# Kernel optimization log

Hardware: AMD Instinct MI355X
Metric: run time of the kernel (lower is better)

## Reference

```python
import jax, jax.numpy as jnp
import numpy as np

VDE, VEN = 30000, 30000
D, H, M = 620, 1000, 1000
B, S, T = 32, 20, 20  # T = decoder steps = y.shape[1]-1


def _lstm(xe, Wih, Whh, b):
    """Single-layer LSTM, batch_first. xe: [B,L,D] -> [B,L,H]. PyTorch gate order i,f,g,o.
    (b = b_ih + b_hh; mathematically identical to PyTorch's two biases.)"""
    Bn = xe.shape[0]
    Hn = Whh.shape[1]
    xp = jnp.einsum('bld,gd->blg', xe, Wih) + b  # [B,L,4H]

    def step(carry, xt):
        h, c = carry
        gates = xt + h @ Whh.T
        i, f, g, o = jnp.split(gates, 4, axis=-1)
        c = jax.nn.sigmoid(f) * c + jax.nn.sigmoid(i) * jnp.tanh(g)
        h = jax.nn.sigmoid(o) * jnp.tanh(c)
        return (h, c), h

    init = (jnp.zeros((Bn, Hn), xe.dtype), jnp.zeros((Bn, Hn), xe.dtype))
    _, hs = jax.lax.scan(step, init, jnp.swapaxes(xp, 0, 1))
    return jnp.swapaxes(hs, 0, 1)


def setup_inputs() -> dict:
    key = jax.random.key(0)
    ks = jax.random.split(key, 24)

    def w(k, shape, s=0.05):
        return jax.random.normal(k, shape, jnp.float32) * s

    return {
        'x': jax.random.randint(ks[0], (B, S), 0, VDE),
        'y': jax.random.randint(ks[1], (B, T + 1), 0, VEN),
        'emb_de': w(ks[2], (VDE, D)),
        'emb_en': w(ks[3], (VEN, D)),
        'enc_Wih': w(ks[4], (4 * H, D)), 'enc_Whh': w(ks[5], (4 * H, H)), 'enc_b': jnp.zeros((4 * H,), jnp.float32),
        'dec_Wih': w(ks[6], (4 * H, D)), 'dec_Whh': w(ks[7], (4 * H, H)), 'dec_b': jnp.zeros((4 * H,), jnp.float32),
        'Wa_w': w(ks[8], (H, H)), 'Wa_b': jnp.zeros((H,), jnp.float32),
        'Ua_w': w(ks[9], (H, H)), 'Ua_b': jnp.zeros((H,), jnp.float32),
        'Va_w': w(ks[10], (H,)), 'Va_b': jnp.zeros((), jnp.float32),
        'U_w': w(ks[11], (2 * M, H)), 'U_b': jnp.zeros((2 * M,), jnp.float32),
        'V_w': w(ks[12], (2 * M, D)), 'V_b': jnp.zeros((2 * M,), jnp.float32),
        'C_w': w(ks[13], (2 * M, H)), 'C_b': jnp.zeros((2 * M,), jnp.float32),
        'W_w': w(ks[14], (VEN, M)), 'W_b': jnp.zeros((VEN,), jnp.float32),
    }


def reference(x, y, emb_de, emb_en, enc_Wih, enc_Whh, enc_b,
              dec_Wih, dec_Whh, dec_b, Wa_w, Wa_b, Ua_w, Ua_b, Va_w, Va_b,
              U_w, U_b, V_w, V_b, C_w, C_b, W_w, W_b):
    e_de = emb_de[x]                 # [B,S,D]
    e_en = emb_en[y]                 # [B,T+1,D]
    enc_h = _lstm(e_de, enc_Wih, enc_Whh, enc_b)          # [B,S,H]
    dec_h = _lstm(e_en[:, :-1], dec_Wih, dec_Whh, dec_b)  # [B,T,H]

    # Bahdanau additive attention (fused broadcast-add + tanh + Va)
    Wa = jnp.einsum('bth,gh->btg', dec_h, Wa_w) + Wa_b    # [B,T,H]
    Ua = jnp.einsum('bsh,gh->bsg', enc_h, Ua_w) + Ua_b    # [B,S,H]
    scores = jnp.einsum('bsth,h->bst', jnp.tanh(Ua[:, :, None, :] + Wa[:, None, :, :]), Va_w) + Va_b  # [B,S,T]

    attn = jax.nn.softmax(scores, axis=1)                 # softmax over source positions
    context = jnp.einsum('bst,bsh->bth', attn, enc_h)     # [B,T,H]

    # deep-output maxout layer, batched over all t
    u = (jnp.einsum('bth,gh->btg', dec_h, U_w) + U_b
         + jnp.einsum('btd,gd->btg', e_en[:, :-1], V_w) + V_b
         + jnp.einsum('bth,gh->btg', context, C_w) + C_b)  # [B,T,2M]
    t_max = jnp.max(u.reshape(B, T, M, 2), axis=-1)        # [B,T,M]

    logits = jnp.einsum('btm,vm->btv', t_max, W_w) + W_b   # [B,T,Ven]
    logp = jax.nn.log_softmax(logits, axis=-1)
    labels = y[:, 1:]                                      # [B,T]
    nll = -jnp.take_along_axis(logp, labels[:, :, None], axis=-1)[..., 0]  # [B,T]
    # original: sum over t of NLLLoss(mean over batch)
    loss = jnp.sum(jnp.mean(nll, axis=0))
    return loss
```

## Files before the change

### kernel.cpp

```cpp
#include <hip/hip_runtime.h>
#include <math.h>

#define VEN_  30000
#define Dd    620
#define Hh    1000
#define Gg    4000
#define Mm    1000
#define Bb    32
#define Ss    20
#define Tt    20
#define NST   470

typedef __attribute__((ext_vector_type(8))) short short8b;
typedef __attribute__((ext_vector_type(4))) float f32x4;

typedef __attribute__((address_space(1))) void GASV;
typedef __attribute__((address_space(3))) void LASV;
#define GLOAD_LDS16(g, l) \
    __builtin_amdgcn_global_load_lds((GASV*)(const void*)(g), (LASV*)(void*)(l), 16, 0, 0)

__device__ __forceinline__ float sigf(float x) { return 1.0f / (1.0f + __expf(-x)); }
__device__ __forceinline__ ushort f2bf(float f) {
    unsigned u = __float_as_uint(f);
    u = (u + 0x7fffu + ((u >> 16) & 1u)) >> 16;
    return (ushort)u;
}
__device__ __forceinline__ float bf2f(ushort u) { return __uint_as_float(((unsigned)u) << 16); }
__device__ __forceinline__ short8b cvt8(float4 a, float4 b) {
    ushort v[8];
    v[0] = f2bf(a.x); v[1] = f2bf(a.y); v[2] = f2bf(a.z); v[3] = f2bf(a.w);
    v[4] = f2bf(b.x); v[5] = f2bf(b.y); v[6] = f2bf(b.z); v[7] = f2bf(b.w);
    return *(short8b*)v;
}

__global__ void conv_bf16(const float* __restrict__ in, int K,
                          ushort* __restrict__ out, int ostride, int kp8, int total) {
    int idx = blockIdx.x * 256 + threadIdx.x;
    if (idx >= total) return;
    int rr = idx / kp8, c8 = (idx % kp8) * 8;
    const float* src = in + (size_t)rr * K + c8;
    short8b o;
    if (c8 + 7 < K) {
        o = cvt8(*(const float4*)src, *(const float4*)(src + 4));
    } else {
        ushort v[8];
        #pragma unroll
        for (int j = 0; j < 8; ++j) v[j] = (c8 + j < K) ? f2bf(src[j]) : (ushort)0;
        o = *(short8b*)v;
    }
    *(short8b*)&out[(size_t)rr * ostride + c8] = o;
}

struct ConvJob { const float* src; ushort* dst; int K; int ostride; int kp8; unsigned end; };
struct ConvJobs { ConvJob j[9]; };

__global__ void conv_multi(ConvJobs jobs, unsigned total) {
    unsigned v = blockIdx.x * 256 + threadIdx.x;
    if (v >= total) return;
    int ji = 0;
    while (v >= jobs.j[ji].end) ++ji;
    unsigned base = ji ? jobs.j[ji - 1].end : 0;
    unsigned local = v - base;
    const ConvJob J = jobs.j[ji];
    int rr = local / J.kp8, c8 = (local % J.kp8) * 8;
    const float* src = J.src + (size_t)rr * J.K + c8;
    short8b o;
    if (c8 + 7 < J.K) {
        o = cvt8(*(const float4*)src, *(const float4*)(src + 4));
    } else {
        ushort w[8];
        #pragma unroll
        for (int j = 0; j < 8; ++j) w[j] = (c8 + j < J.K) ? f2bf(src[j]) : (ushort)0;
        o = *(short8b*)w;
    }
    *(short8b*)&J.dst[(size_t)rr * J.ostride + c8] = o;
}

__global__ void gather2(const float* __restrict__ embA, const int* __restrict__ tokA,
                        int strA, ushort* __restrict__ outA, int osA,
                        const float* __restrict__ embB, const int* __restrict__ tokB,
                        int strB, ushort* __restrict__ outB, int osB) {
    int idx = blockIdx.x * 256 + threadIdx.x;
    if (idx >= Bb * Tt * 80) return;
    const float* emb; const int* toks; int tstride; ushort* out; int ostride;
    if (blockIdx.y == 0) { emb = embA; toks = tokA; tstride = strA; out = outA; ostride = osA; }
    else                 { emb = embB; toks = tokB; tstride = strB; out = outB; ostride = osB; }
    int row = idx / 80, c8 = (idx % 80) * 8;
    int b = row / Tt, t = row % Tt;
    int tok = toks[b * tstride + t];
    const float* src = emb + (size_t)tok * Dd + c8;
    short8b o;
    if (c8 + 7 < Dd) {
        o = cvt8(*(const float4*)src, *(const float4*)(src + 4));
    } else {
        ushort v[8];
        #pragma unroll
        for (int j = 0; j < 8; ++j) v[j] = (c8 + j < Dd) ? f2bf(src[j]) : (ushort)0;
        o = *(short8b*)v;
    }
    *(short8b*)&out[(size_t)row * ostride + c8] = o;
}

struct GemmArgs {
    const ushort* A; int lda;
    const ushort* B; int ldb;
    const float* bias; const float* bias2; const float* bias3;
    float* C; int ldc;
    float* pm; float* ps; ushort* Cb;
    int M, N, Kp, MT;
};

template <int MODE>
__device__ __forceinline__ void gemm_body(ushort* As, ushort* Bs, const GemmArgs g) {
    const int tid = threadIdx.x;
    const int w = tid >> 6, lane = tid & 63;
    const int wm = w >> 1, wn = w & 1;
    const int lhi = lane >> 4, llo = lane & 15;

    int nblk = gridDim.x;
    int q = nblk >> 3, r = nblk & 7;
    int xcd = blockIdx.x & 7, lo = blockIdx.x >> 3;
    int wg = ((xcd < r) ? xcd * (q + 1) : r * (q + 1) + (xcd - r) * q) + lo;
    int mt = wg % g.MT, nt = wg / g.MT;
    const int row0 = mt * 128, col0 = nt * 128;

    const int lr8 = lane >> 3;
    const int cs = (lane & 7) ^ lr8;
    const ushort* pA[4];
    const ushort* pB[4];
    #pragma unroll
    for (int qq = 0; qq < 4; ++qq) {
        int seg = w + qq * 4;
        int ra = row0 + seg * 8 + lr8; if (ra > g.M - 1) ra = g.M - 1;
        int rb = col0 + seg * 8 + lr8; if (rb > g.N - 1) rb = g.N - 1;
        pA[qq] = g.A + (size_t)ra * g.lda + cs * 8;
        pB[qq] = g.B + (size_t)rb * g.ldb + cs * 8;
    }

    f32x4 acc[4][4] = {};

    #pragma unroll
    for (int qq = 0; qq < 4; ++qq) {
        int seg = w + qq * 4;
        GLOAD_LDS16(pA[qq], (char*)As + (seg << 10));
        GLOAD_LDS16(pB[qq], (char*)Bs + (seg << 10));
    }
    __syncthreads();

    int cur = 0;
    for (int kk = 0; kk < g.Kp; kk += 64) {
        if (kk + 64 < g.Kp) {
            int nb = (cur ^ 1) << 14;
            #pragma unroll
            for (int qq = 0; qq < 4; ++qq) {
                int seg = w + qq * 4;
                GLOAD_LDS16(pA[qq] + kk + 64, (char*)As + nb + (seg << 10));
                GLOAD_LDS16(pB[qq] + kk + 64, (char*)Bs + nb + (seg << 10));
            }
        }
        const char* curA = (const char*)As + (cur << 14);
        const char* curB = (const char*)Bs + (cur << 14);
        #pragma unroll
        for (int ks = 0; ks < 2; ++ks) {
            short8b af[4], bg[4];
            #pragma unroll
            for (int i = 0; i < 4; ++i) {
                int Ra = wm * 64 + i * 16 + llo;
                int ca = (ks * 4 + lhi) ^ (Ra & 7);
                af[i] = *(const short8b*)(curA + Ra * 128 + (ca << 4));
                int Rb = wn * 64 + i * 16 + llo;
                int cbs = (ks * 4 + lhi) ^ (Rb & 7);
                bg[i] = *(const short8b*)(curB + Rb * 128 + (cbs << 4));
            }
            #pragma unroll
            for (int i = 0; i < 4; ++i)
                #pragma unroll
                for (int j = 0; j < 4; ++j)
                    acc[i][j] = __builtin_amdgcn_mfma_f32_16x16x32_bf16(af[i], bg[j], acc[i][j], 0, 0, 0);
        }
        __syncthreads();
        cur ^= 1;
    }

    if (MODE == 0) {
        #pragma unroll
        for (int i = 0; i < 4; ++i) {
            #pragma unroll
            for (int reg = 0; reg < 4; ++reg) {
                int row = row0 + wm * 64 + i * 16 + lhi * 4 + reg;
                if (row >= g.M) continue;
                #pragma unroll
                for (int j = 0; j < 4; ++j) {
                    int col = col0 + wn * 64 + j * 16 + llo;
                    if (col < g.N)
                        g.C[(size_t)row * g.ldc + col] = acc[i][j][reg] + (g.bias ? g.bias[col] : 0.f);
                }
            }
        }
    } else if (MODE == 1) {
        #pragma unroll
        for (int i = 0; i < 4; ++i) {
            #pragma unroll
            for (int reg = 0; reg < 4; ++reg) {
                int row = row0 + wm * 64 + i * 16 + lhi * 4 + reg;
                float vals[4], vmax = -1e30f;
                #pragma unroll
                for (int j = 0; j < 4; ++j) {
                    int col = col0 + wn * 64 + j * 16 + llo;
                    vals[j] = (col < g.N) ? (acc[i][j][reg] + g.bias[col]) : -1e30f;
                    vmax = fmaxf(vmax, vals[j]);
                }
                #pragma unroll
                for (int off = 8; off; off >>= 1) vmax = fmaxf(vmax, __shfl_xor(vmax, off, 16));
                float se = 0.f;
                #pragma unroll
                for (int j = 0; j < 4; ++j) {
                    int col = col0 + wn * 64 + j * 16 + llo;
                    if (col < g.N) se += __expf(vals[j] - vmax);
                }
                #pragma unroll
                for (int off = 8; off; off >>= 1) se += __shfl_xor(se, off, 16);
                if (llo == 0 && row < g.M) {
                    g.pm[(size_t)row * NST + nt * 2 + wn] = vmax;
                    g.ps[(size_t)row * NST + nt * 2 + wn] = se;
                }
            }
        }
    } else {
        #pragma unroll
        for (int i = 0; i < 4; ++i) {
            #pragma unroll
            for (int reg = 0; reg < 4; ++reg) {
                int row = row0 + wm * 64 + i * 16 + lhi * 4 + reg;
                #pragma unroll
                for (int j = 0; j < 4; ++j) {
                    int col = col0 + wn * 64 + j * 16 + llo;
                    int cc = col < g.N ? col : 0;
                    float bv = g.bias[cc] + (g.bias2 ? g.bias2[cc] : 0.f) + (g.bias3 ? g.bias3[cc] : 0.f);
                    float v = acc[i][j][reg] + bv;
                    float o = fmaxf(v, __shfl_xor(v, 1));
                    if (((llo & 1) == 0) && row < g.M && col + 1 < g.N) {
                        int m = col >> 1;
                        g.C[(size_t)row * g.ldc + m] = o;
                        g.Cb[(size_t)row * 1024 + m] = f2bf(o);
                    }
                }
            }
        }
    }
}

template <int MODE>
__global__ __launch_bounds__(256) void gemm_one(GemmArgs g) {
    __shared__ __align__(16) ushort As[2 * 128 * 64];
    __shared__ __align__(16) ushort Bs[2 * 128 * 64];
    gemm_body<MODE>(As, Bs, g);
}

__global__ __launch_bounds__(256) void gemm_pair(GemmArgs g0, GemmArgs g1) {
    __shared__ __align__(16) ushort As[2 * 128 * 64];
    __shared__ __align__(16) ushort Bs[2 * 128 * 64];
    if (blockIdx.y == 0) gemm_body<0>(As, Bs, g0);
    else                 gemm_body<0>(As, Bs, g1);
}

__global__ __launch_bounds__(512) void lstm_all(
    const float* __restrict__ xpE, const float* __restrict__ xpD,
    const ushort* __restrict__ WE, const ushort* __restrict__ WD,
    ushort* __restrict__ hE, ushort* __restrict__ hD,
    int strideE, int strideD, unsigned* __restrict__ flags)
{
    __shared__ float gsm[8][32][16];
    const int which = blockIdx.y;
    const float* xp = which ? xpD : xpE;
    const ushort* Whh = which ? WD : WE;
    ushort* hs = which ? hD : hE;
    const int hstride = which ? strideD : strideE;
    unsigned* fl = flags + which * 64;

    const int tid = threadIdx.x;
    const int wave = tid >> 6, l = tid & 63;
    const int g = wave & 3, half = wave >> 2;
    const int lhi = l >> 4, llo = l & 15;
    const int j0 = blockIdx.x * 16;
    const int jc = (j0 + llo < Hh) ? (j0 + llo) : (Hh - 1);
    const int kbase = half * 512;
    const ushort* wp = Whh + (size_t)(g * Hh + jc) * 1024 + kbase + lhi * 8;

    short8b wreg[16];
    #pragma unroll
    for (int kk = 0; kk < 16; ++kk) wreg[kk] = *(const short8b*)(wp + kk * 32);

    const int ub = tid >> 4, ujj = tid & 15;
    const int ujw = j0 + ujj;
    const float* xpr = xp + (size_t)ub * Tt * Gg;
    float creg = 0.f;

    for (int t = 0; t < Tt; ++t) {
        f32x4 acc0 = {0.f, 0.f, 0.f, 0.f};
        f32x4 acc1 = {0.f, 0.f, 0.f, 0.f};
        if (t > 0) {
            const ushort* h0p = hs + ((size_t)llo * Tt + (t - 1)) * hstride + kbase + lhi * 8;
            const ushort* h1p = hs + ((size_t)(llo + 16) * Tt + (t - 1)) * hstride + kbase + lhi * 8;
            short8b a0r[4], a1r[4];
            #pragma unroll
            for (int pp = 0; pp < 4; ++pp) {
                a0r[pp] = *(const short8b*)(h0p + pp * 32);
                a1r[pp] = *(const short8b*)(h1p + pp * 32);
            }
            #pragma unroll
            for (int kk = 0; kk < 16; ++kk) {
                short8b a0 = a0r[kk & 3], a1 = a1r[kk & 3];
                if (kk + 4 < 16) {
                    a0r[kk & 3] = *(const short8b*)(h0p + (kk + 4) * 32);
                    a1r[kk & 3] = *(const short8b*)(h1p + (kk + 4) * 32);
                }
                acc0 = __builtin_amdgcn_mfma_f32_16x16x32_bf16(a0, wreg[kk], acc0, 0, 0, 0);
                acc1 = __builtin_amdgcn_mfma_f32_16x16x32_bf16(a1, wreg[kk], acc1, 0, 0, 0);
            }
        }
        #pragma unroll
        for (int reg = 0; reg < 4; ++reg) {
            gsm[wave][lhi * 4 + reg][llo]      = acc0[reg];
            gsm[wave][16 + lhi * 4 + reg][llo] = acc1[reg];
        }
        __syncthreads();
        {
            const float* xq = xpr + (size_t)t * Gg;
            float hn = 0.f;
            if (ujw < Hh) {
                float vi = gsm[0][ub][ujj] + gsm[4][ub][ujj] + xq[ujw];
                float vf = gsm[1][ub][ujj] + gsm[5][ub][ujj] + xq[Hh + ujw];
                float vg = gsm[2][ub][ujj] + gsm[6][ub][ujj] + xq[2 * Hh + ujw];
                float vo = gsm[3][ub][ujj] + gsm[7][ub][ujj] + xq[3 * Hh + ujw];
                creg = sigf(vf) * creg + sigf(vi) * tanhf(vg);
                hn = sigf(vo) * tanhf(creg);
            }
            unsigned mine = f2bf(hn);
            unsigned other = (unsigned)__shfl_xor((int)mine, 1);
            if (((ujj & 1) == 0) && ujw + 1 < Hh + 1 && ujw < Hh) {
                unsigned pk = (other << 16) | (mine & 0xFFFFu);
                unsigned* dst = (unsigned*)&hs[((size_t)ub * Tt + t) * hstride + ujw];
                __hip_atomic_store(dst, pk, __ATOMIC_RELAXED, __HIP_MEMORY_SCOPE_SYSTEM);
            }
        }
        if (t + 1 < Tt) {
            __syncthreads();
            if (tid == 0)
                __hip_atomic_store(&fl[blockIdx.x], (unsigned)(t + 1),
                                   __ATOMIC_RELAXED, __HIP_MEMORY_SCOPE_SYSTEM);
            if (tid < 64) {
                unsigned tgt = (unsigned)(t + 1);
                while (true) {
                    unsigned v = (tid < 63)
                        ? __hip_atomic_load(&fl[tid], __ATOMIC_RELAXED, __HIP_MEMORY_SCOPE_SYSTEM)
                        : tgt;
                    if (__all(v >= tgt)) break;
                    __builtin_amdgcn_s_sleep(1);
                }
            }
            __syncthreads();
        }
    }
}

__global__ __launch_bounds__(256) void attn_scores(
    const float* __restrict__ Ua, const float* __restrict__ Wa,
    const float* __restrict__ Va_w, const float* __restrict__ Va_b,
    float* __restrict__ scores)
{
    int wave = (blockIdx.x * 256 + threadIdx.x) >> 6;
    int lane = threadIdx.x & 63;
    if (wave >= Bb * Ss * Tt) return;
    int b = wave / (Ss * Tt);
    int rem = wave % (Ss * Tt);
    int s = rem / Tt, t = rem % Tt;
    const float* ua = Ua + (size_t)(b * Ss + s) * Hh;
    const float* wa = Wa + (size_t)(b * Tt + t) * Hh;
    float acc = 0.f;
    for (int h = lane; h < Hh; h += 64)
        acc += tanhf(ua[h] + wa[h]) * Va_w[h];
    #pragma unroll
    for (int off = 32; off; off >>= 1) acc += __shfl_xor(acc, off, 64);
    if (lane == 0) scores[(size_t)(b * Ss + s) * Tt + t] = acc + Va_b[0];
}

__global__ __launch_bounds__(256) void softmax_context(
    const float* __restrict__ scores, const ushort* __restrict__ enc_hb,
    ushort* __restrict__ ctx_out, int ostride)
{
    __shared__ float w[Ss];
    int b = blockIdx.x / Tt, t = blockIdx.x % Tt;
    if (threadIdx.x == 0) {
        float sc[Ss];
        float mx = -1e30f;
        for (int s = 0; s < Ss; ++s) {
            sc[s] = scores[(size_t)(b * Ss + s) * Tt + t];
            mx = fmaxf(mx, sc[s]);
        }
        float sum = 0.f;
        for (int s = 0; s < Ss; ++s) { float e = __expf(sc[s] - mx); w[s] = e; sum += e; }
        float inv = 1.f / sum;
        for (int s = 0; s < Ss; ++s) w[s] *= inv;
    }
    __syncthreads();
    for (int h = threadIdx.x; h < Hh; h += 256) {
        float acc = 0.f;
        #pragma unroll
        for (int s = 0; s < Ss; ++s)
            acc += w[s] * bf2f(enc_hb[((size_t)b * Ss + s) * 1024 + h]);
        ctx_out[(size_t)(b * Tt + t) * ostride + h] = f2bf(acc);
    }
}

__global__ __launch_bounds__(256) void nll_kernel(
    const float* __restrict__ pm, const float* __restrict__ ps,
    const float* __restrict__ tmax, const float* __restrict__ Ww,
    const float* __restrict__ Wb, const int* __restrict__ y,
    float* __restrict__ nll)
{
    __shared__ float sm[4];
    int row = blockIdx.x;
    int tid = threadIdx.x;
    float mx = -1e30f;
    for (int i = tid; i < NST; i += 256) mx = fmaxf(mx, pm[(size_t)row * NST + i]);
    #pragma unroll
    for (int off = 32; off; off >>= 1) mx = fmaxf(mx, __shfl_xor(mx, off, 64));
    if ((tid & 63) == 0) sm[tid >> 6] = mx;
    __syncthreads();
    mx = fmaxf(fmaxf(sm[0], sm[1]), fmaxf(sm[2], sm[3]));
    __syncthreads();
    float s = 0.f;
    for (int i = tid; i < NST; i += 256)
        s += ps[(size_t)row * NST + i] * __expf(pm[(size_t)row * NST + i] - mx);
    #pragma unroll
    for (int off = 32; off; off >>= 1) s += __shfl_xor(s, off, 64);
    if ((tid & 63) == 0) sm[tid >> 6] = s;
    __syncthreads();
    s = sm[0] + sm[1] + sm[2] + sm[3];
    __syncthreads();
    int b = row / Tt, t = row % Tt;
    int lab = y[b * (Tt + 1) + t + 1];
    float d = 0.f;
    for (int m = tid; m < Mm; m += 256)
        d += tmax[(size_t)row * Mm + m] * Ww[(size_t)lab * Mm + m];
    #pragma unroll
    for (int off = 32; off; off >>= 1) d += __shfl_xor(d, off, 64);
    if ((tid & 63) == 0) sm[tid >> 6] = d;
    __syncthreads();
    d = sm[0] + sm[1] + sm[2] + sm[3] + Wb[lab];
    if (tid == 0) nll[row] = (mx + logf(s)) - d;
}

__global__ void loss_kernel(const float* __restrict__ nll, float* __restrict__ out) {
    __shared__ float sm[4];
    float s = 0.f;
    for (int i = threadIdx.x; i < Bb * Tt; i += 256) s += nll[i];
    #pragma unroll
    for (int off = 32; off; off >>= 1) s += __shfl_xor(s, off, 64);
    if ((threadIdx.x & 63) == 0) sm[threadIdx.x >> 6] = s;
    __syncthreads();
    if (threadIdx.x == 0) out[0] = (sm[0] + sm[1] + sm[2] + sm[3]) / (float)Bb;
}

extern "C" void kernel_launch(void* const* d_in, const int* in_sizes, int n_in,
                              void* d_out, int out_size, void* d_ws, size_t ws_size,
                              hipStream_t stream)
{
    const int* x = (const int*)d_in[0];
    const int* y = (const int*)d_in[1];
    const float* emb_de  = (const float*)d_in[2];
    const float* emb_en  = (const float*)d_in[3];
    const float* enc_Wih = (const float*)d_in[4];
    const float* enc_Whh = (const float*)d_in[5];
    const float* enc_b   = (const float*)d_in[6];
    const float* dec_Wih = (const float*)d_in[7];
    const float* dec_Whh = (const float*)d_in[8];
    const float* dec_b   = (const float*)d_in[9];
    const float* Wa_w = (const float*)d_in[10];
    const float* Wa_b = (const float*)d_in[11];
    const float* Ua_w = (const float*)d_in[12];
    const float* Ua_b = (const float*)d_in[13];
    const float* Va_w = (const float*)d_in[14];
    const float* Va_b = (const float*)d_in[15];
    const float* U_w  = (const float*)d_in[16];
    const float* U_b  = (const float*)d_in[17];
    const float* V_w  = (const float*)d_in[18];
    const float* V_b  = (const float*)d_in[19];
    const float* C_w  = (const float*)d_in[20];
    const float* C_b  = (const float*)d_in[21];
    const float* W_w  = (const float*)d_in[22];
    const float* W_b  = (const float*)d_in[23];

    char* base = (char*)d_ws;
    size_t off = 0;
    auto alloc = [&](size_t bytes) { char* p = base + off; off += (bytes + 255) & ~(size_t)255; return p; };

    float*  xp_enc   = (float*)alloc(640ull * 4000 * 4);
    float*  xp_dec   = (float*)alloc(640ull * 4000 * 4);
    float*  Wa       = (float*)alloc(640ull * 1000 * 4);
    float*  Ua       = (float*)alloc(640ull * 1000 * 4);
    float*  scores   = (float*)alloc((size_t)Bb * Ss * Tt * 4);
    float*  pm       = (float*)alloc(640ull * NST * 4);
    float*  ps       = (float*)alloc(640ull * NST * 4);
    float*  nll      = (float*)alloc(640ull * 4);
    ushort* e_de_b   = (ushort*)alloc(640ull * 640 * 2);
    ushort* A_cat    = (ushort*)alloc(640ull * 2688 * 2);
    ushort* hs_enc_b = (ushort*)alloc(640ull * 1024 * 2);
    unsigned* flags  = (unsigned*)alloc(512);
    ushort* whh_enc_b= (ushort*)alloc(4000ull * 1024 * 2);
    ushort* whh_dec_b= (ushort*)alloc(4000ull * 1024 * 2);
    ushort* wbig     = (ushort*)alloc(30000ull * 1024 * 2);
    ushort* Wcat_b   = (ushort*)alloc(2000ull * 2688 * 2);
    ushort* Wa_w_b   = (ushort*)alloc(1000ull * 1024 * 2);
    ushort* Ua_w_b   = (ushort*)alloc(1000ull * 1024 * 2);

    ushort* wih_enc_b = wbig;
    ushort* wih_dec_b = wbig + 4000ull * 640;
    ushort* W_w_b     = wbig;

    float*  tmax   = xp_enc + 640ull * 2000;
    ushort* tmax_b = (ushort*)xp_dec;

    dim3 blk(256);

    hipMemsetAsync(A_cat, 0, 640ull * 2688 * 2 + 640ull * 1024 * 2 + 512, stream);

    ConvJobs jobs;
    unsigned acc = 0;
    auto J = [&](int i, const float* s, ushort* d, int K, int ostr, int kp8, int R) {
        acc += (unsigned)R * kp8;
        jobs.j[i] = ConvJob{s, d, K, ostr, kp8, acc};
    };
    J(0, enc_Whh, whh_enc_b, 1000, 1024, 128, 4000);
    J(1, dec_Whh, whh_dec_b, 1000, 1024, 128, 4000);
    J(2, enc_Wih, wih_enc_b,  620,  640,  80, 4000);
    J(3, dec_Wih, wih_dec_b,  620,  640,  80, 4000);
    J(4, Wa_w,    Wa_w_b,    1000, 1024, 128, 1000);
    J(5, Ua_w,    Ua_w_b,    1000, 1024, 128, 1000);
    J(6, U_w,     Wcat_b,          1000, 2688, 128, 2000);
    J(7, V_w,     Wcat_b + 1024,    620, 2688,  80, 2000);
    J(8, C_w,     Wcat_b + 1664,   1000, 2688, 128, 2000);
    conv_multi<<<dim3((acc + 255) / 256), blk, 0, stream>>>(jobs, acc);

    gather2<<<dim3(200, 2), blk, 0, stream>>>(emb_de, x, Ss, e_de_b, 640,
                                              emb_en, y, Tt + 1, A_cat + 1024, 2688);

    GemmArgs ge = {e_de_b, 640, wih_enc_b, 640, enc_b, nullptr, nullptr,
                   xp_enc, 4000, nullptr, nullptr, nullptr, 640, 4000, 640, 5};
    GemmArgs gd = {A_cat + 1024, 2688, wih_dec_b, 640, dec_b, nullptr, nullptr,
                   xp_dec, 4000, nullptr, nullptr, nullptr, 640, 4000, 640, 5};
    gemm_pair<<<dim3(160, 2), blk, 0, stream>>>(ge, gd);

    conv_bf16<<<dim3(15000), blk, 0, stream>>>(W_w, 1000, W_w_b, 1024, 128, 30000 * 128);

    lstm_all<<<dim3(63, 2), dim3(512), 0, stream>>>(
        xp_enc, xp_dec, whh_enc_b, whh_dec_b, hs_enc_b, A_cat, 1024, 2688, flags);

    GemmArgs gw = {A_cat, 2688, Wa_w_b, 1024, Wa_b, nullptr, nullptr,
                   Wa, 1000, nullptr, nullptr, nullptr, 640, 1000, 1024, 5};
    GemmArgs gu = {hs_enc_b, 1024, Ua_w_b, 1024, Ua_b, nullptr, nullptr,
                   Ua, 1000, nullptr, nullptr, nullptr, 640, 1000, 1024, 5};
    gemm_pair<<<dim3(40, 2), blk, 0, stream>>>(gw, gu);

    attn_scores<<<dim3(3200), blk, 0, stream>>>(Ua, Wa, Va_w, Va_b, scores);
    softmax_context<<<dim3(640), blk, 0, stream>>>(scores, hs_enc_b, A_cat + 1664, 2688);

    hipMemsetAsync(tmax_b, 0, 640ull * 1024 * 2, stream);

    GemmArgs gm = {A_cat, 2688, Wcat_b, 2688, U_b, V_b, C_b,
                   tmax, 1000, nullptr, nullptr, tmax_b, 640, 2000, 2688, 5};
    gemm_one<2><<<dim3(80), blk, 0, stream>>>(gm);

    GemmArgs gl = {tmax_b, 1024, W_w_b, 1024, W_b, nullptr, nullptr,
                   nullptr, 0, pm, ps, nullptr, 640, VEN_, 1024, 5};
    gemm_one<1><<<dim3(1175), blk, 0, stream>>>(gl);

    nll_kernel<<<dim3(640), blk, 0, stream>>>(pm, ps, tmax, W_w, W_b, y, nll);
    loss_kernel<<<dim3(1), blk, 0, stream>>>(nll, (float*)d_out);
}
```

Measured before the change: 514.3 us.

## Overlap W_w bf16 conversion with LSTM recurrence inside one launch

Removes the standalone conv_bf16 launch. The fp32-to-bf16 conversion of the large output projection W_w is folded into lstm_all as extra worker blocks (6 of every 8 blocks), so it runs alongside the latency-bound recurrent blocks instead of before them. It also prefetches the xp gate inputs before the MFMA work, reads h through agent-scope relaxed atomic loads, and narrows the store and flag atomics from system to agent scope to make cross-block syncs cheaper. The risk is that the conversion blocks compete with the spin-waiting recurrence blocks for bandwidth and CU slots, and residency of all recurrence blocks now depends on the 504-block grid scheduling.

```diff
diff --git a/kernel.cpp b/kernel.cpp
--- a/kernel.cpp
+++ b/kernel.cpp
@@ -31,24 +31,6 @@
     v[0] = f2bf(a.x); v[1] = f2bf(a.y); v[2] = f2bf(a.z); v[3] = f2bf(a.w);
     v[4] = f2bf(b.x); v[5] = f2bf(b.y); v[6] = f2bf(b.z); v[7] = f2bf(b.w);
     return *(short8b*)v;
-}
-
-__global__ void conv_bf16(const float* __restrict__ in, int K,
-                          ushort* __restrict__ out, int ostride, int kp8, int total) {
-    int idx = blockIdx.x * 256 + threadIdx.x;
-    if (idx >= total) return;
-    int rr = idx / kp8, c8 = (idx % kp8) * 8;
-    const float* src = in + (size_t)rr * K + c8;
-    short8b o;
-    if (c8 + 7 < K) {
-        o = cvt8(*(const float4*)src, *(const float4*)(src + 4));
-    } else {
-        ushort v[8];
-        #pragma unroll
-        for (int j = 0; j < 8; ++j) v[j] = (c8 + j < K) ? f2bf(src[j]) : (ushort)0;
-        o = *(short8b*)v;
-    }
-    *(short8b*)&out[(size_t)rr * ostride + c8] = o;
 }
 
 struct ConvJob { const float* src; ushort* dst; int K; int ostride; int kp8; unsigned end; };
@@ -264,14 +246,39 @@
     else                 gemm_body<0>(As, Bs, g1);
 }
 
+union HQ { unsigned long long q[2]; short8b v; };
+
 __global__ __launch_bounds__(512) void lstm_all(
     const float* __restrict__ xpE, const float* __restrict__ xpD,
     const ushort* __restrict__ WE, const ushort* __restrict__ WD,
     ushort* __restrict__ hE, ushort* __restrict__ hD,
-    int strideE, int strideD, unsigned* __restrict__ flags)
+    int strideE, int strideD, unsigned* __restrict__ flags,
+    const float* __restrict__ Ww, ushort* __restrict__ Wwb)
 {
+    const int role = blockIdx.x & 7;
+    const int chunk = blockIdx.x >> 3;
+    if (role != 0 && role != 4) {
+        int wid = chunk * 6 + (role < 4 ? role - 1 : role - 2);
+        const int total = 30000 * 128;
+        for (int idx = wid * 512 + (int)threadIdx.x; idx < total; idx += 378 * 512) {
+            int rr = idx >> 7, c8 = (idx & 127) * 8;
+            const float* src = Ww + (size_t)rr * 1000 + c8;
+            short8b o;
+            if (c8 + 7 < 1000) {
+                o = cvt8(*(const float4*)src, *(const float4*)(src + 4));
+            } else {
+                ushort v[8];
+                #pragma unroll
+                for (int j = 0; j < 8; ++j) v[j] = (c8 + j < 1000) ? f2bf(src[j]) : (ushort)0;
+                o = *(short8b*)v;
+            }
+            *(short8b*)&Wwb[(size_t)rr * 1024 + c8] = o;
+        }
+        return;
+    }
+
     __shared__ float gsm[8][32][16];
-    const int which = blockIdx.y;
+    const int which = role >> 2;
     const float* xp = which ? xpD : xpE;
     const ushort* Whh = which ? WD : WE;
     ushort* hs = which ? hD : hE;
@@ -282,7 +289,7 @@
     const int wave = tid >> 6, l = tid & 63;
     const int g = wave & 3, half = wave >> 2;
     const int lhi = l >> 4, llo = l & 15;
-    const int j0 = blockIdx.x * 16;
+    const int j0 = chunk * 16;
     const int jc = (j0 + llo < Hh) ? (j0 + llo) : (Hh - 1);
     const int kbase = half * 512;
     const ushort* wp = Whh + (size_t)(g * Hh + jc) * 1024 + kbase + lhi * 8;
@@ -297,23 +304,35 @@
     float creg = 0.f;
 
     for (int t = 0; t < Tt; ++t) {
+        float xq0 = 0.f, xq1 = 0.f, xq2 = 0.f, xq3 = 0.f;
+        if (ujw < Hh) {
+            const float* xq = xpr + (size_t)t * Gg;
+            xq0 = xq[ujw]; xq1 = xq[Hh + ujw]; xq2 = xq[2 * Hh + ujw]; xq3 = xq[3 * Hh + ujw];
+        }
+
         f32x4 acc0 = {0.f, 0.f, 0.f, 0.f};
         f32x4 acc1 = {0.f, 0.f, 0.f, 0.f};
         if (t > 0) {
-            const ushort* h0p = hs + ((size_t)llo * Tt + (t - 1)) * hstride + kbase + lhi * 8;
-            const ushort* h1p = hs + ((size_t)(llo + 16) * Tt + (t - 1)) * hstride + kbase + lhi * 8;
-            short8b a0r[4], a1r[4];
+            const unsigned long long* h0q = (const unsigned long long*)
+                (hs + ((size_t)llo * Tt + (t - 1)) * hstride + kbase + lhi * 8);
+            const unsigned long long* h1q = (const unsigned long long*)
+                (hs + ((size_t)(llo + 16) * Tt + (t - 1)) * hstride + kbase + lhi * 8);
+            HQ a0r[4], a1r[4];
             #pragma unroll
             for (int pp = 0; pp < 4; ++pp) {
-                a0r[pp] = *(const short8b*)(h0p + pp * 32);
-                a1r[pp] = *(const short8b*)(h1p + pp * 32);
+                a0r[pp].q[0] = __hip_atomic_load(h0q + pp * 8,     __ATOMIC_RELAXED, __HIP_MEMORY_SCOPE_AGENT);
+                a0r[pp].q[1] = __hip_atomic_load(h0q + pp * 8 + 1, __ATOMIC_RELAXED, __HIP_MEMORY_SCOPE_AGENT);
+                a1r[pp].q[0] = __hip_atomic_load(h1q + pp * 8,     __ATOMIC_RELAXED, __HIP_MEMORY_SCOPE_AGENT);
+                a1r[pp].q[1] = __hip_atomic_load(h1q + pp * 8 + 1, __ATOMIC_RELAXED, __HIP_MEMORY_SCOPE_AGENT);
             }
             #pragma unroll
             for (int kk = 0; kk < 16; ++kk) {
-                short8b a0 = a0r[kk & 3], a1 = a1r[kk & 3];
+                short8b a0 = a0r[kk & 3].v, a1 = a1r[kk & 3].v;
                 if (kk + 4 < 16) {
-                    a0r[kk & 3] = *(const short8b*)(h0p + (kk + 4) * 32);
-                    a1r[kk & 3] = *(const short8b*)(h1p + (kk + 4) * 32);
+                    a0r[kk & 3].q[0] = __hip_atomic_load(h0q + (kk + 4) * 8,     __ATOMIC_RELAXED, __HIP_MEMORY_SCOPE_AGENT);
+                    a0r[kk & 3].q[1] = __hip_atomic_load(h0q + (kk + 4) * 8 + 1, __ATOMIC_RELAXED, __HIP_MEMORY_SCOPE_AGENT);
+                    a1r[kk & 3].q[0] = __hip_atomic_load(h1q + (kk + 4) * 8,     __ATOMIC_RELAXED, __HIP_MEMORY_SCOPE_AGENT);
+                    a1r[kk & 3].q[1] = __hip_atomic_load(h1q + (kk + 4) * 8 + 1, __ATOMIC_RELAXED, __HIP_MEMORY_SCOPE_AGENT);
                 }
                 acc0 = __builtin_amdgcn_mfma_f32_16x16x32_bf16(a0, wreg[kk], acc0, 0, 0, 0);
                 acc1 = __builtin_amdgcn_mfma_f32_16x16x32_bf16(a1, wreg[kk], acc1, 0, 0, 0);
@@ -326,34 +345,33 @@
         }
         __syncthreads();
         {
-            const float* xq = xpr + (size_t)t * Gg;
             float hn = 0.f;
             if (ujw < Hh) {
-                float vi = gsm[0][ub][ujj] + gsm[4][ub][ujj] + xq[ujw];
-                float vf = gsm[1][ub][ujj] + gsm[5][ub][ujj] + xq[Hh + ujw];
-                float vg = gsm[2][ub][ujj] + gsm[6][ub][ujj] + xq[2 * Hh + ujw];
-                float vo = gsm[3][ub][ujj] + gsm[7][ub][ujj] + xq[3 * Hh + ujw];
+                float vi = gsm[0][ub][ujj] + gsm[4][ub][ujj] + xq0;
+                float vf = gsm[1][ub][ujj] + gsm[5][ub][ujj] + xq1;
+                float vg = gsm[2][ub][ujj] + gsm[6][ub][ujj] + xq2;
+                float vo = gsm[3][ub][ujj] + gsm[7][ub][ujj] + xq3;
                 creg = sigf(vf) * creg + sigf(vi) * tanhf(vg);
                 hn = sigf(vo) * tanhf(creg);
             }
             unsigned mine = f2bf(hn);
             unsigned other = (unsigned)__shfl_xor((int)mine, 1);
-            if (((ujj & 1) == 0) && ujw + 1 < Hh + 1 && ujw < Hh) {
+            if (((ujj & 1) == 0) && ujw < Hh) {
                 unsigned pk = (other << 16) | (mine & 0xFFFFu);
                 unsigned* dst = (unsigned*)&hs[((size_t)ub * Tt + t) * hstride + ujw];
-                __hip_atomic_store(dst, pk, __ATOMIC_RELAXED, __HIP_MEMORY_SCOPE_SYSTEM);
+                __hip_atomic_store(dst, pk, __ATOMIC_RELAXED, __HIP_MEMORY_SCOPE_AGENT);
             }
         }
         if (t + 1 < Tt) {
             __syncthreads();
             if (tid == 0)
-                __hip_atomic_store(&fl[blockIdx.x], (unsigned)(t + 1),
-                                   __ATOMIC_RELAXED, __HIP_MEMORY_SCOPE_SYSTEM);
+                __hip_atomic_store(&fl[chunk], (unsigned)(t + 1),
+                                   __ATOMIC_RELAXED, __HIP_MEMORY_SCOPE_AGENT);
             if (tid < 64) {
                 unsigned tgt = (unsigned)(t + 1);
                 while (true) {
                     unsigned v = (tid < 63)
-                        ? __hip_atomic_load(&fl[tid], __ATOMIC_RELAXED, __HIP_MEMORY_SCOPE_SYSTEM)
+                        ? __hip_atomic_load(&fl[tid], __ATOMIC_RELAXED, __HIP_MEMORY_SCOPE_AGENT)
                         : tgt;
                     if (__all(v >= tgt)) break;
                     __builtin_amdgcn_s_sleep(1);
@@ -552,10 +570,9 @@
                    xp_dec, 4000, nullptr, nullptr, nullptr, 640, 4000, 640, 5};
     gemm_pair<<<dim3(160, 2), blk, 0, stream>>>(ge, gd);
 
-    conv_bf16<<<dim3(15000), blk, 0, stream>>>(W_w, 1000, W_w_b, 1024, 128, 30000 * 128);
-
-    lstm_all<<<dim3(63, 2), dim3(512), 0, stream>>>(
-        xp_enc, xp_dec, whh_enc_b, whh_dec_b, hs_enc_b, A_cat, 1024, 2688, flags);
+    lstm_all<<<dim3(504), dim3(512), 0, stream>>>(
+        xp_enc, xp_dec, whh_enc_b, whh_dec_b, hs_enc_b, A_cat, 1024, 2688, flags,
+        W_w, W_w_b);
 
     GemmArgs gw = {A_cat, 2688, Wa_w_b, 1024, Wa_b, nullptr, nullptr,
                    Wa, 1000, nullptr, nullptr, nullptr, 640, 1000, 1024, 5};
```

New measurement: 941.7 us. 83.1% more time.

## Fold gathers and W_w conversion into conv_multi, fuse loss reduction, drop memset

Applied to the files above, without the earlier changes.

Adds token-indexed gather jobs to the multi-job conversion kernel so the separate gather launch goes away. When the workspace is large enough, the W_w bf16 conversion gets its own buffer and joins the same launch. The final loss reduction moves into nll_kernel via a last-block atomic counter, and the tmax_b memset is replaced by the maxout GEMM writing zeros into the padding itself. The LSTM spin-wait sleep is raised from 1 to 8, which trades polling traffic against wake-up latency.

```diff
diff --git a/kernel.cpp b/kernel.cpp
--- a/kernel.cpp
+++ b/kernel.cpp
@@ -51,8 +51,11 @@
     *(short8b*)&out[(size_t)rr * ostride + c8] = o;
 }
 
-struct ConvJob { const float* src; ushort* dst; int K; int ostride; int kp8; unsigned end; };
-struct ConvJobs { ConvJob j[9]; };
+struct ConvJob {
+    const float* src; ushort* dst; const int* tok;
+    unsigned end; int K; int ostride; int kp8; int tstride;
+};
+struct ConvJobs { ConvJob j[12]; };
 
 __global__ void conv_multi(ConvJobs jobs, unsigned total) {
     unsigned v = blockIdx.x * 256 + threadIdx.x;
@@ -63,7 +66,9 @@
     unsigned local = v - base;
     const ConvJob J = jobs.j[ji];
     int rr = local / J.kp8, c8 = (local % J.kp8) * 8;
-    const float* src = J.src + (size_t)rr * J.K + c8;
+    int srow = rr;
+    if (J.tok) srow = J.tok[(rr / Tt) * J.tstride + (rr % Tt)];
+    const float* src = J.src + (size_t)srow * J.K + c8;
     short8b o;
     if (c8 + 7 < J.K) {
         o = cvt8(*(const float4*)src, *(const float4*)(src + 4));
@@ -74,31 +79,6 @@
         o = *(short8b*)w;
     }
     *(short8b*)&J.dst[(size_t)rr * J.ostride + c8] = o;
-}
-
-__global__ void gather2(const float* __restrict__ embA, const int* __restrict__ tokA,
-                        int strA, ushort* __restrict__ outA, int osA,
-                        const float* __restrict__ embB, const int* __restrict__ tokB,
-                        int strB, ushort* __restrict__ outB, int osB) {
-    int idx = blockIdx.x * 256 + threadIdx.x;
-    if (idx >= Bb * Tt * 80) return;
-    const float* emb; const int* toks; int tstride; ushort* out; int ostride;
-    if (blockIdx.y == 0) { emb = embA; toks = tokA; tstride = strA; out = outA; ostride = osA; }
-    else                 { emb = embB; toks = tokB; tstride = strB; out = outB; ostride = osB; }
-    int row = idx / 80, c8 = (idx % 80) * 8;
-    int b = row / Tt, t = row % Tt;
-    int tok = toks[b * tstride + t];
-    const float* src = emb + (size_t)tok * Dd + c8;
-    short8b o;
-    if (c8 + 7 < Dd) {
-        o = cvt8(*(const float4*)src, *(const float4*)(src + 4));
-    } else {
-        ushort v[8];
-        #pragma unroll
-        for (int j = 0; j < 8; ++j) v[j] = (c8 + j < Dd) ? f2bf(src[j]) : (ushort)0;
-        o = *(short8b*)v;
-    }
-    *(short8b*)&out[(size_t)row * ostride + c8] = o;
 }
 
 struct GemmArgs {
@@ -239,10 +219,14 @@
                     float bv = g.bias[cc] + (g.bias2 ? g.bias2[cc] : 0.f) + (g.bias3 ? g.bias3[cc] : 0.f);
                     float v = acc[i][j][reg] + bv;
                     float o = fmaxf(v, __shfl_xor(v, 1));
-                    if (((llo & 1) == 0) && row < g.M && col + 1 < g.N) {
+                    if (((llo & 1) == 0) && row < g.M) {
                         int m = col >> 1;
-                        g.C[(size_t)row * g.ldc + m] = o;
-                        g.Cb[(size_t)row * 1024 + m] = f2bf(o);
+                        if (col + 1 < g.N) {
+                            g.C[(size_t)row * g.ldc + m] = o;
+                            g.Cb[(size_t)row * 1024 + m] = f2bf(o);
+                        } else if (col >= g.N && m < 1024) {
+                            g.Cb[(size_t)row * 1024 + m] = 0;
+                        }
                     }
                 }
             }
@@ -338,7 +322,7 @@
             }
             unsigned mine = f2bf(hn);
             unsigned other = (unsigned)__shfl_xor((int)mine, 1);
-            if (((ujj & 1) == 0) && ujw + 1 < Hh + 1 && ujw < Hh) {
+            if (((ujj & 1) == 0) && ujw < Hh) {
                 unsigned pk = (other << 16) | (mine & 0xFFFFu);
                 unsigned* dst = (unsigned*)&hs[((size_t)ub * Tt + t) * hstride + ujw];
                 __hip_atomic_store(dst, pk, __ATOMIC_RELAXED, __HIP_MEMORY_SCOPE_SYSTEM);
@@ -356,7 +340,7 @@
                         ? __hip_atomic_load(&fl[tid], __ATOMIC_RELAXED, __HIP_MEMORY_SCOPE_SYSTEM)
                         : tgt;
                     if (__all(v >= tgt)) break;
-                    __builtin_amdgcn_s_sleep(1);
+                    __builtin_amdgcn_s_sleep(8);
                 }
             }
             __syncthreads();
@@ -417,9 +401,11 @@
     const float* __restrict__ pm, const float* __restrict__ ps,
     const float* __restrict__ tmax, const float* __restrict__ Ww,
     const float* __restrict__ Wb, const int* __restrict__ y,
-    float* __restrict__ nll)
+    float* __restrict__ nll, unsigned* __restrict__ ready,
+    float* __restrict__ out)
 {
     __shared__ float sm[4];
+    __shared__ unsigned lastf;
     int row = blockIdx.x;
     int tid = threadIdx.x;
     float mx = -1e30f;
@@ -449,18 +435,23 @@
     if ((tid & 63) == 0) sm[tid >> 6] = d;
     __syncthreads();
     d = sm[0] + sm[1] + sm[2] + sm[3] + Wb[lab];
-    if (tid == 0) nll[row] = (mx + logf(s)) - d;
-}
-
-__global__ void loss_kernel(const float* __restrict__ nll, float* __restrict__ out) {
-    __shared__ float sm[4];
-    float s = 0.f;
-    for (int i = threadIdx.x; i < Bb * Tt; i += 256) s += nll[i];
-    #pragma unroll
-    for (int off = 32; off; off >>= 1) s += __shfl_xor(s, off, 64);
-    if ((threadIdx.x & 63) == 0) sm[threadIdx.x >> 6] = s;
-    __syncthreads();
-    if (threadIdx.x == 0) out[0] = (sm[0] + sm[1] + sm[2] + sm[3]) / (float)Bb;
+    if (tid == 0) {
+        float v = (mx + logf(s)) - d;
+        __hip_atomic_store(&nll[row], v, __ATOMIC_RELAXED, __HIP_MEMORY_SCOPE_SYSTEM);
+        asm volatile("s_waitcnt vmcnt(0)" ::: "memory");
+        lastf = __hip_atomic_fetch_add(ready, 1u, __ATOMIC_RELAXED, __HIP_MEMORY_SCOPE_AGENT);
+    }
+    __syncthreads();
+    if (lastf == (unsigned)(Bb * Tt - 1)) {
+        float acc = 0.f;
+        for (int i = tid; i < Bb * Tt; i += 256)
+            acc += __hip_atomic_load(&nll[i], __ATOMIC_RELAXED, __HIP_MEMORY_SCOPE_SYSTEM);
+        #pragma unroll
+        for (int off = 32; off; off >>= 1) acc += __shfl_xor(acc, off, 64);
+        if ((tid & 63) == 0) sm[tid >> 6] = acc;
+        __syncthreads();
+        if (tid == 0) out[0] = (sm[0] + sm[1] + sm[2] + sm[3]) / (float)Bb;
+    }
 }
 
 extern "C" void kernel_launch(void* const* d_in, const int* in_sizes, int n_in,
@@ -517,34 +508,44 @@
 
     ushort* wih_enc_b = wbig;
     ushort* wih_dec_b = wbig + 4000ull * 640;
-    ushort* W_w_b     = wbig;
+
+    ushort* W_w_b = wbig;
+    bool sepWw = (ws_size >= off + 30000ull * 1024 * 2 + 256);
+    if (sepWw) W_w_b = (ushort*)alloc(30000ull * 1024 * 2);
 
     float*  tmax   = xp_enc + 640ull * 2000;
     ushort* tmax_b = (ushort*)xp_dec;
+    unsigned* ready = &flags[120];
 
     dim3 blk(256);
 
     hipMemsetAsync(A_cat, 0, 640ull * 2688 * 2 + 640ull * 1024 * 2 + 512, stream);
 
-    ConvJobs jobs;
+    ConvJobs jobs = {};
     unsigned acc = 0;
-    auto J = [&](int i, const float* s, ushort* d, int K, int ostr, int kp8, int R) {
+    int nj = 0;
+    auto JC = [&](const float* s, ushort* d, int K, int ostr, int kp8, int R) {
         acc += (unsigned)R * kp8;
-        jobs.j[i] = ConvJob{s, d, K, ostr, kp8, acc};
+        jobs.j[nj++] = ConvJob{s, d, nullptr, acc, K, ostr, kp8, 0};
     };
-    J(0, enc_Whh, whh_enc_b, 1000, 1024, 128, 4000);
-    J(1, dec_Whh, whh_dec_b, 1000, 1024, 128, 4000);
-    J(2, enc_Wih, wih_enc_b,  620,  640,  80, 4000);
-    J(3, dec_Wih, wih_dec_b,  620,  640,  80, 4000);
-    J(4, Wa_w,    Wa_w_b,    1000, 1024, 128, 1000);
-    J(5, Ua_w,    Ua_w_b,    1000, 1024, 128, 1000);
-    J(6, U_w,     Wcat_b,          1000, 2688, 128, 2000);
-    J(7, V_w,     Wcat_b + 1024,    620, 2688,  80, 2000);
-    J(8, C_w,     Wcat_b + 1664,   1000, 2688, 128, 2000);
+    auto JG = [&](const float* emb, ushort* d, const int* tok, int tstr, int ostr) {
+        acc += 640u * 80;
+        jobs.j[nj++] = ConvJob{emb, d, tok, acc, Dd, ostr, 80, tstr};
+    };
+    JC(enc_Whh, whh_enc_b, 1000, 1024, 128, 4000);
+    JC(dec_Whh, whh_dec_b, 1000, 1024, 128, 4000);
+    JC(enc_Wih, wih_enc_b,  620,  640,  80, 4000);
+    JC(dec_Wih, wih_dec_b,  620,  640,  80, 4000);
+    JC(Wa_w,    Wa_w_b,    1000, 1024, 128, 1000);
+    JC(Ua_w,    Ua_w_b,    1000, 1024, 128, 1000);
+    JC(U_w,     Wcat_b,          1000, 2688, 128, 2000);
+    JC(V_w,     Wcat_b + 1024,    620, 2688,  80, 2000);
+    JC(C_w,     Wcat_b + 1664,   1000, 2688, 128, 2000);
+    JG(emb_de, e_de_b,       x, Ss,     640);
+    JG(emb_en, A_cat + 1024, y, Tt + 1, 2688);
+    if (sepWw) JC(W_w, W_w_b, 1000, 1024, 128, 30000);
+    for (int i = nj; i < 12; ++i) jobs.j[i].end = acc;
     conv_multi<<<dim3((acc + 255) / 256), blk, 0, stream>>>(jobs, acc);
-
-    gather2<<<dim3(200, 2), blk, 0, stream>>>(emb_de, x, Ss, e_de_b, 640,
-                                              emb_en, y, Tt + 1, A_cat + 1024, 2688);
 
     GemmArgs ge = {e_de_b, 640, wih_enc_b, 640, enc_b, nullptr, nullptr,
                    xp_enc, 4000, nullptr, nullptr, nullptr, 640, 4000, 640, 5};
@@ -552,7 +553,8 @@
                    xp_dec, 4000, nullptr, nullptr, nullptr, 640, 4000, 640, 5};
     gemm_pair<<<dim3(160, 2), blk, 0, stream>>>(ge, gd);
 
-    conv_bf16<<<dim3(15000), blk, 0, stream>>>(W_w, 1000, W_w_b, 1024, 128, 30000 * 128);
+    if (!sepWw)
+        conv_bf16<<<dim3(15000), blk, 0, stream>>>(W_w, 1000, W_w_b, 1024, 128, 30000 * 128);
 
     lstm_all<<<dim3(63, 2), dim3(512), 0, stream>>>(
         xp_enc, xp_dec, whh_enc_b, whh_dec_b, hs_enc_b, A_cat, 1024, 2688, flags);
@@ -566,8 +568,6 @@
     attn_scores<<<dim3(3200), blk, 0, stream>>>(Ua, Wa, Va_w, Va_b, scores);
     softmax_context<<<dim3(640), blk, 0, stream>>>(scores, hs_enc_b, A_cat + 1664, 2688);
 
-    hipMemsetAsync(tmax_b, 0, 640ull * 1024 * 2, stream);
-
     GemmArgs gm = {A_cat, 2688, Wcat_b, 2688, U_b, V_b, C_b,
                    tmax, 1000, nullptr, nullptr, tmax_b, 640, 2000, 2688, 5};
     gemm_one<2><<<dim3(80), blk, 0, stream>>>(gm);
@@ -576,6 +576,6 @@
                    nullptr, 0, pm, ps, nullptr, 640, VEN_, 1024, 5};
     gemm_one<1><<<dim3(1175), blk, 0, stream>>>(gl);
 
-    nll_kernel<<<dim3(640), blk, 0, stream>>>(pm, ps, tmax, W_w, W_b, y, nll);
-    loss_kernel<<<dim3(1), blk, 0, stream>>>(nll, (float*)d_out);
-}
+    nll_kernel<<<dim3(640), blk, 0, stream>>>(pm, ps, tmax, W_w, W_b, y,
+                                              nll, ready, (float*)d_out);
+}
```

Result: no change. 519.8 us (+1.1%).
